# Kernel optimization log

Measured on AMD Instinct MI355X. Metric: run time of the kernel, lower is better.

The kernel has to match this reference:

```python
import jax, jax.numpy as jnp
from jax import lax
import numpy as np

_BN_SCALE = 1.0 / float(np.sqrt(1.0 + 1e-5))  # eval BN: running_mean=0, running_var=1
SEMANTIC_GROUPS = [
    ("head_spine", [0, 1, 2, 3, 20]),
    ("left_arm", [4, 5, 6, 7, 21, 22]),
    ("right_arm", [8, 9, 10, 11, 23, 24]),
    ("left_leg", [12, 13, 14, 15]),
    ("right_leg", [16, 17, 18, 19]),
]
_SKELETON_EDGES = [(3, 2), (2, 20), (20, 1), (1, 0), (20, 4), (4, 5), (5, 6), (6, 22), (6, 7), (7, 21),
                   (20, 8), (8, 9), (9, 10), (10, 24), (10, 11), (11, 23), (0, 12), (12, 13), (13, 14),
                   (14, 15), (0, 16), (16, 17), (17, 18), (18, 19)]


def _full_adj():
    adj = np.zeros((25, 25))
    for i, j in [(a - 1, b - 1) for a, b in _SKELETON_EDGES]:
        if 0 <= i < 25 and 0 <= j < 25:
            adj[i, j] = 1.0
            adj[j, i] = 1.0
    adj += np.eye(25)
    deg = adj.sum(1, keepdims=True)
    deg[deg == 0] = 1.0
    return adj / deg


def _sub_adj(joints):
    fa = _full_adj()
    sa = fa[np.ix_(joints, joints)].copy()
    n = len(joints)
    if n > 1:
        sa += np.eye(n)
        deg = sa.sum(1)
        for node in np.nonzero(deg == 1.0)[0]:
            if node != 0:
                sa[0, node] = 1.0
                sa[node, 0] = 1.0
    deg = sa.sum(1, keepdims=True)
    deg[deg == 0] = 1.0
    return jnp.asarray((sa / deg).astype(np.float32))


def _bn(y, g, b):
    # eval-mode BatchNorm2d with running stats (0, 1)
    return y * (g * _BN_SCALE)[None, :, None, None] + b[None, :, None, None]


def _st_layer(x, adj, sw, sb, tw, tb, g, b, res):
    # x: (B, Cin, T, V); sw: (3*Cout, Cin); tw: (Cout, Cout, 3, 1)
    if res is None:
        r = x
    else:
        rw, rb, rg, rbb = res
        r = _bn(jnp.einsum('oc,bctv->botv', rw, x) + rb[None, :, None, None], rg, rbb)
    xg = jnp.einsum('uv,bctv->bctu', adj, x)  # adjacency message passing
    y = jnp.einsum('oc,bctv->botv', sw, xg) + sb[None, :, None, None]
    B, oc3, T, V = y.shape
    y = y.reshape(B, 3, oc3 // 3, T, V).sum(axis=1)  # sum spatial kernel partitions
    y = lax.conv_general_dilated(y, tw, (1, 1), ((1, 1), (0, 0))) + tb[None, :, None, None]
    return jax.nn.relu(_bn(y + r, g, b))


def _vq(inp, cb):
    # inp: (B, D), cb: (K, D); straight-through VQ with commitment_cost=0.25
    d = jnp.sum(inp * inp, 1, keepdims=True) + jnp.sum(cb * cb, 1) - 2.0 * (inp @ cb.T)
    idx = jnp.argmin(d, axis=1)
    q = cb[idx]
    sg = lax.stop_gradient
    loss = jnp.mean((q - sg(inp)) ** 2) + 0.25 * jnp.mean((sg(q) - inp) ** 2)
    return inp + sg(q - inp), loss, idx


def _forward(x, embed_w, embed_b, p1, p2, p3, codebooks):
    h = jnp.einsum('btvc,oc->btvo', x, embed_w) + embed_b  # (B,T,25,64)
    h = h.transpose(0, 3, 1, 2)  # (B,64,T,25)
    quants, losses, idxs = [], [], []
    for gi, (_, joints) in enumerate(SEMANTIC_GROUPS):
        adj = _sub_adj(joints)
        y = h[:, :, :, np.asarray(joints)]
        sw1, sb1, tw1, tb1, g1, b1 = [p[gi] for p in p1]
        y = _st_layer(y, adj, sw1, sb1, tw1, tb1, g1, b1, None)
        rw2, rb2, rg2, rbb2, sw2, sb2, tw2, tb2, g2, b2 = [p[gi] for p in p2]
        y = _st_layer(y, adj, sw2, sb2, tw2, tb2, g2, b2, (rw2, rb2, rg2, rbb2))
        rw3, rb3, rg3, rbb3, sw3, sb3, tw3, tb3, g3, b3 = [p[gi] for p in p3]
        y = _st_layer(y, adj, sw3, sb3, tw3, tb3, g3, b3, (rw3, rb3, rg3, rbb3))
        feat = y.mean(axis=(2, 3))  # AdaptiveAvgPool2d((1,1))
        q, l, i = _vq(feat, codebooks[gi])
        quants.append(q)
        losses.append(l)
        idxs.append(i)
    return jnp.stack(quants), jnp.sum(jnp.stack(losses)), jnp.stack(idxs)


def setup_inputs() -> dict:
    ks = iter(jax.random.split(jax.random.key(0), 48))

    def rn(shape, scale=0.05):
        return jax.random.normal(next(ks), shape, jnp.float32) * scale

    return {
        "x": jax.random.normal(next(ks), (64, 256, 25, 3), jnp.float32),
        "embed_w": rn((64, 3), 0.3),
        "embed_b": rn((64,), 0.01),
        "sgcn_w1": rn((5, 192, 64)),
        "sgcn_b1": rn((5, 192), 0.01),
        "tconv_w1": rn((5, 64, 64, 3, 1)),
        "tconv_b1": rn((5, 64), 0.01),
        "bn_g1": jnp.ones((5, 64), jnp.float32),
        "bn_b1": jnp.zeros((5, 64), jnp.float32),
        "res_w2": rn((5, 128, 64)),
        "res_b2": rn((5, 128), 0.01),
        "resbn_g2": jnp.ones((5, 128), jnp.float32),
        "resbn_b2": jnp.zeros((5, 128), jnp.float32),
        "sgcn_w2": rn((5, 384, 64)),
        "sgcn_b2": rn((5, 384), 0.01),
        "tconv_w2": rn((5, 128, 128, 3, 1)),
        "tconv_b2": rn((5, 128), 0.01),
        "bn_g2": jnp.ones((5, 128), jnp.float32),
        "bn_b2": jnp.zeros((5, 128), jnp.float32),
        "res_w3": rn((5, 64, 128)),
        "res_b3": rn((5, 64), 0.01),
        "resbn_g3": jnp.ones((5, 64), jnp.float32),
        "resbn_b3": jnp.zeros((5, 64), jnp.float32),
        "sgcn_w3": rn((5, 192, 128)),
        "sgcn_b3": rn((5, 192), 0.01),
        "tconv_w3": rn((5, 64, 64, 3, 1)),
        "tconv_b3": rn((5, 64), 0.01),
        "bn_g3": jnp.ones((5, 64), jnp.float32),
        "bn_b3": jnp.zeros((5, 64), jnp.float32),
        "codebooks": jax.random.uniform(next(ks), (5, 128, 64), jnp.float32, -1.0 / 128, 1.0 / 128),
    }


def reference(x, embed_w, embed_b, sgcn_w1, sgcn_b1, tconv_w1, tconv_b1, bn_g1, bn_b1,
              res_w2, res_b2, resbn_g2, resbn_b2, sgcn_w2, sgcn_b2, tconv_w2, tconv_b2, bn_g2, bn_b2,
              res_w3, res_b3, resbn_g3, resbn_b3, sgcn_w3, sgcn_b3, tconv_w3, tconv_b3, bn_g3, bn_b3,
              codebooks):
    p1 = (sgcn_w1, sgcn_b1, tconv_w1, tconv_b1, bn_g1, bn_b1)
    p2 = (res_w2, res_b2, resbn_g2, resbn_b2, sgcn_w2, sgcn_b2, tconv_w2, tconv_b2, bn_g2, bn_b2)
    p3 = (res_w3, res_b3, resbn_g3, resbn_b3, sgcn_w3, sgcn_b3, tconv_w3, tconv_b3, bn_g3, bn_b3)
    return _forward(x, embed_w, embed_b, p1, p2, p3, codebooks)
```

## Files before the change

### kernel.cpp

```cpp
#include <hip/hip_runtime.h>

#define T_ 256
#define B_ 64
static constexpr float BNS = 0.9999950000374997f;

__device__ __constant__ int d_perm[25] = {0,1,2,3,20, 4,5,6,7,21,22, 8,9,10,11,23,24, 12,13,14,15, 16,17,18,19};
__device__ __constant__ int d_gstart[5] = {0,5,11,17,21};
__device__ __constant__ int d_gn[5] = {5,6,6,4,4};
__device__ __constant__ int d_edges[21][2] = {
  {2,1},{1,19},{19,0},{19,3},{3,4},{4,5},{5,21},{5,6},{6,20},{19,7},
  {7,8},{8,9},{9,23},{9,10},{10,22},{11,12},{12,13},{13,14},{15,16},{16,17},{17,18}};

__global__ void adj_kernel(float* __restrict__ adjout){
  if (threadIdx.x != 0 || blockIdx.x != 0) return;
  double fa[25][25];
  for (int i=0;i<25;i++) for (int j=0;j<25;j++) fa[i][j]=0.0;
  for (int e=0;e<21;e++){ int i=d_edges[e][0], j=d_edges[e][1]; fa[i][j]=1.0; fa[j][i]=1.0; }
  for (int i=0;i<25;i++) fa[i][i] += 1.0;
  for (int i=0;i<25;i++){
    double dg=0; for (int j=0;j<25;j++) dg += fa[i][j];
    if (dg==0.0) dg=1.0;
    for (int j=0;j<25;j++) fa[i][j] /= dg;
  }
  for (int g=0; g<5; g++){
    int n = d_gn[g]; int gs = d_gstart[g];
    for (int q=0;q<36;q++) adjout[g*36+q] = 0.f;
    double sa[6][6];
    for (int a=0;a<n;a++) for (int b=0;b<n;b++) sa[a][b] = fa[d_perm[gs+a]][d_perm[gs+b]];
    for (int a=0;a<n;a++) sa[a][a] += 1.0;
    double deg[6];
    for (int a=0;a<n;a++){ double s=0; for (int b=0;b<n;b++) s += sa[a][b]; deg[a]=s; }
    for (int a=1;a<n;a++) if (deg[a]==1.0){ sa[0][a]=1.0; sa[a][0]=1.0; }
    for (int a=0;a<n;a++){
      double s=0; for (int b=0;b<n;b++) s += sa[a][b];
      if (s==0.0) s=1.0;
      for (int b=0;b<n;b++) adjout[g*36 + a*n + b] = (float)(sa[a][b]/s);
    }
  }
}

__global__ void zero_kernel(float* __restrict__ feat, float* __restrict__ loss){
  int i = blockIdx.x*256 + threadIdx.x;
  if (i < 5*64*64) feat[i] = 0.f;
  if (i == 0) loss[0] = 0.f;
}

__global__ __launch_bounds__(256) void fold_swe(
    const float* __restrict__ sw1, const float* __restrict__ sw2, const float* __restrict__ sw3,
    float* __restrict__ swe1, float* __restrict__ swe2, float* __restrict__ swe3){
  int i = blockIdx.x*256 + threadIdx.x;
  if (i < 20480){ int g=i/4096, r=i%4096;
    swe1[i] = sw1[g*12288 + r] + sw1[g*12288 + 4096 + r] + sw1[g*12288 + 8192 + r];
  } else if (i < 61440){ int j=i-20480; int g=j/8192, r=j%8192;
    swe2[j] = sw2[g*24576 + r] + sw2[g*24576 + 8192 + r] + sw2[g*24576 + 16384 + r];
  } else if (i < 102400){ int j=i-61440; int g=j/8192, r=j%8192;
    swe3[j] = sw3[g*24576 + r] + sw3[g*24576 + 8192 + r] + sw3[g*24576 + 16384 + r];
  }
}

template<int Cm, int Cout>
__global__ __launch_bounds__(256) void transpose_tw(const float* __restrict__ tw, float* __restrict__ twT){
  int e = blockIdx.x*256 + threadIdx.x;
  if (e >= 5*3*Cm*Cout) return;
  int o = e % Cout;
  int t = e / Cout;
  int m = t % Cm; t /= Cm;
  int k = t % 3; int g = t/3;
  twT[e] = tw[(size_t)g*Cout*Cm*3 + (o*Cm+m)*3 + k];
}

template<int Cm, int Cin, int Cout>
__global__ __launch_bounds__(256) void prep_gemm(
    const float* __restrict__ twT, const float* __restrict__ swe,
    const float* __restrict__ bg, float* __restrict__ WC){
  constexpr int CT = 256/Cout;
  __shared__ float sS[Cm*CT];
  int g = blockIdx.x, k = blockIdx.y, cz = blockIdx.z;
  int tid = threadIdx.x;
  for (int i=tid; i<Cm*CT; i+=256){
    int m = i/CT, cc = i%CT;
    sS[i] = swe[(size_t)g*Cm*Cin + m*Cin + cz*CT + cc];
  }
  __syncthreads();
  int o = tid % Cout, cc = tid / Cout;
  const float* tp = twT + ((size_t)(g*3+k)*Cm)*Cout + o;
  float acc = 0.f;
  #pragma unroll 4
  for (int m=0;m<Cm;m++) acc += tp[(size_t)m*Cout]*sS[m*CT+cc];
  int c = cz*CT + cc;
  WC[(size_t)g*3*Cin*Cout + ((size_t)k*Cin + c)*Cout + o] = bg[g*Cout+o]*BNS*acc;
}

__global__ __launch_bounds__(256) void prep_rw(
    const float* __restrict__ rw2, const float* __restrict__ rg2, const float* __restrict__ bg2,
    const float* __restrict__ rw3, const float* __restrict__ rg3, const float* __restrict__ bg3,
    float* __restrict__ RW2, float* __restrict__ RW3){
  int i = blockIdx.x*256 + threadIdx.x;
  if (i < 40960){ int g=i/8192, r=i%8192, c=r>>7, o=r&127;
    RW2[i] = bg2[g*128+o]*BNS*rg2[g*128+o]*BNS*rw2[(size_t)g*8192 + o*64 + c];
  } else if (i < 81920){ int j=i-40960; int g=j/8192, r=j%8192, c=r>>6, o=r&63;
    RW3[j] = bg3[g*64+o]*BNS*rg3[g*64+o]*BNS*rw3[(size_t)g*8192 + o*128 + c];
  }
}

__global__ __launch_bounds__(128) void prep_bias(
    const float* __restrict__ twT1, const float* __restrict__ twT2, const float* __restrict__ twT3,
    const float* __restrict__ sb1, const float* __restrict__ tb1, const float* __restrict__ bg1, const float* __restrict__ bb1,
    const float* __restrict__ sb2, const float* __restrict__ tb2, const float* __restrict__ bg2, const float* __restrict__ bb2,
    const float* __restrict__ rb2, const float* __restrict__ rg2, const float* __restrict__ rbb2,
    const float* __restrict__ sb3, const float* __restrict__ tb3, const float* __restrict__ bg3, const float* __restrict__ bb3,
    const float* __restrict__ rb3, const float* __restrict__ rg3, const float* __restrict__ rbb3,
    float* __restrict__ B1, float* __restrict__ RS1, float* __restrict__ B2, float* __restrict__ B3){
  __shared__ float sbe[128];
  int g = blockIdx.x, L = blockIdx.y, tid = threadIdx.x;
  if (L == 0){
    if (tid<64) sbe[tid] = sb1[g*192+tid] + sb1[g*192+64+tid] + sb1[g*192+128+tid];
    __syncthreads();
    if (tid<64){ int o=tid; float gsc = bg1[g*64+o]*BNS;
      for (int k=0;k<3;k++){ float s=0.f; const float* tp = twT1 + ((size_t)(g*3+k)*64)*64 + o;
        for (int m=0;m<64;m++) s += tp[m*64]*sbe[m];
        B1[g*256+(k+1)*64+o] = gsc*s; }
      B1[g*256+o] = gsc*tb1[g*64+o] + bb1[g*64+o];
      RS1[g*64+o] = gsc;
    }
  } else if (L == 1){
    sbe[tid] = sb2[g*384+tid] + sb2[g*384+128+tid] + sb2[g*384+256+tid];
    __syncthreads();
    { int o=tid; float gsc = bg2[g*128+o]*BNS; float rgs = rg2[g*128+o]*BNS;
      for (int k=0;k<3;k++){ float s=0.f; const float* tp = twT2 + ((size_t)(g*3+k)*128)*128 + o;
        for (int m=0;m<128;m++) s += tp[m*128]*sbe[m];
        B2[g*512+(k+1)*128+o] = gsc*s; }
      B2[g*512+o] = gsc*(tb2[g*128+o] + rgs*rb2[g*128+o] + rbb2[g*128+o]) + bb2[g*128+o];
    }
  } else {
    if (tid<64) sbe[tid] = sb3[g*192+tid] + sb3[g*192+64+tid] + sb3[g*192+128+tid];
    __syncthreads();
    if (tid<64){ int o=tid; float gsc = bg3[g*64+o]*BNS; float rgs = rg3[g*64+o]*BNS;
      for (int k=0;k<3;k++){ float s=0.f; const float* tp = twT3 + ((size_t)(g*3+k)*64)*64 + o;
        for (int m=0;m<64;m++) s += tp[m*64]*sbe[m];
        B3[g*256+(k+1)*64+o] = gsc*s; }
      B3[g*256+o] = gsc*(tb3[g*64+o] + rgs*rb3[g*64+o] + rbb3[g*64+o]) + bb3[g*64+o];
    }
  }
}

template<int Cin, int COS, int NJ, int MODE>
__global__ __launch_bounds__(256) void st_layer(
    const float* __restrict__ in, float* __restrict__ out,
    const float* __restrict__ W, const float* __restrict__ RW,
    const float* __restrict__ BV, const float* __restrict__ RS,
    const float* __restrict__ adjg, const float* __restrict__ ew,
    const float* __restrict__ eb, int gstart)
{
  constexpr int TC = 16;
  constexpr int SE = (TC+2)*NJ;
  constexpr int SITES = TC*NJ;
  constexpr int SP = SITES/8;
  static_assert(SP == 2*NJ, "tap-merge ranges assume SP == 2*NJ (TC=16)");
  constexpr int OP = 2;
  constexpr int NCH = Cin/32;
  constexpr int G = (SP%4==0) ? 4 : 5;
  __shared__ float sIn[SE*32];
  __shared__ float sXg[SE*32];
  __shared__ float sAdj[NJ*NJ];
  __shared__ float sX3[MODE==1 ? SE*3 : 1];
  const int tid = threadIdx.x;
  const int b = blockIdx.y;
  const int t0 = blockIdx.x*TC;
  const int ooff = blockIdx.z*64;
  W += ooff; BV += ooff;
  if (MODE != 1) RW += ooff;
  if (MODE == 2) out += ooff;

  if (tid < NJ*NJ) sAdj[tid] = adjg[tid];
  if (MODE == 1){
    for (int e=tid; e<SE*3; e+=256){
      int se = e/3, j = e - se*3;
      int tl = se/NJ; int u = se - tl*NJ; int t = t0 + tl - 1;
      float v = 0.f;
      if (t>=0 && t<T_){ int joint = d_perm[gstart+u]; v = in[(((size_t)b*T_ + t)*25 + joint)*3 + j]; }
      sX3[e] = v;
    }
  }

  const int lane = tid & 63;
  const int o = lane & 31;
  const int sg = (tid>>6)*2 + (lane>>5);
  const int s0 = sg*SP;

  float acc[SP][OP];
  {
    float bno[OP], bk0[OP], bk1[OP], bk2[OP];
    #pragma unroll
    for (int j=0;j<OP;j++){ int oj = j*32 + o;
      bno[j]=BV[oj]; bk0[j]=BV[COS+oj]; bk1[j]=BV[2*COS+oj]; bk2[j]=BV[3*COS+oj]; }
    #pragma unroll
    for (int i=0;i<SP;i++){
      int s = s0 + i; int tg = t0 + s/NJ;
      #pragma unroll
      for (int j=0;j<OP;j++)
        acc[i][j] = bno[j] + bk1[j] + (tg>0 ? bk0[j] : 0.f) + (tg<T_-1 ? bk2[j] : 0.f);
    }
  }

  #pragma unroll 1
  for (int cz=0; cz<NCH; ++cz){
    __syncthreads();
    if (MODE == 1){
      int cg = cz*32 + (tid & 31);
      float w0 = ew[cg*3], w1 = ew[cg*3+1], w2 = ew[cg*3+2], b0 = eb[cg];
      for (int e=tid; e<SE*32; e+=256){
        int se = e>>5; int t = t0 + se/NJ - 1;
        float v = 0.f;
        if (t>=0 && t<T_) v = b0 + sX3[se*3]*w0 + sX3[se*3+1]*w1 + sX3[se*3+2]*w2;
        sIn[e] = v;
      }
    } else {
      for (int e4=tid; e4<SE*8; e4+=256){
        int se = e4>>3; int cc = (e4&7)<<2;
        int tl = se/NJ; int u = se - tl*NJ; int t = t0 + tl - 1;
        float4 v = make_float4(0.f,0.f,0.f,0.f);
        if (t>=0 && t<T_) v = *(const float4*)&in[(((size_t)b*T_ + t)*NJ + u)*(size_t)Cin + cz*32 + cc];
        *(float4*)&sIn[se*32+cc] = v;
      }
    }
    __syncthreads();
    for (int e=tid; e<SE*32; e+=256){
      int se = e>>5; int c = e&31; int u = se%NJ; int base = (se-u)*32 + c;
      float a = 0.f;
      #pragma unroll
      for (int v=0; v<NJ; v++) a += sAdj[u*NJ+v]*sIn[base + v*32];
      sXg[e] = a;
    }
    __syncthreads();
    #pragma unroll 1
    for (int c4=0;c4<32;c4+=4){
      const float* Wc = W + (size_t)(cz*32 + c4)*COS;
      float wv[3][4][OP];
      #pragma unroll
      for (int k=0;k<3;k++)
        #pragma unroll
        for (int q=0;q<4;q++)
          #pragma unroll
          for (int j=0;j<OP;j++)
            wv[k][q][j] = Wc[((size_t)k*Cin + q)*COS + j*32 + o];
      {
        float4 xr[NJ];
        #pragma unroll
        for (int r=0;r<NJ;r++) xr[r] = *(const float4*)&sXg[(s0+r)*32 + c4];
        #pragma unroll
        for (int r=0;r<NJ;r++)
          #pragma unroll
          for (int j=0;j<OP;j++)
            acc[r][j] += xr[r].x*wv[0][0][j] + xr[r].y*wv[0][1][j] + xr[r].z*wv[0][2][j] + xr[r].w*wv[0][3][j];
      }
      {
        float4 xr[NJ];
        #pragma unroll
        for (int r=0;r<NJ;r++) xr[r] = *(const float4*)&sXg[(s0+NJ+r)*32 + c4];
        #pragma unroll
        for (int r=0;r<NJ;r++){
          #pragma unroll
          for (int j=0;j<OP;j++)
            acc[NJ+r][j] += xr[r].x*wv[0][0][j] + xr[r].y*wv[0][1][j] + xr[r].z*wv[0][2][j] + xr[r].w*wv[0][3][j];
          #pragma unroll
          for (int j=0;j<OP;j++)
            acc[r][j] += xr[r].x*wv[1][0][j] + xr[r].y*wv[1][1][j] + xr[r].z*wv[1][2][j] + xr[r].w*wv[1][3][j];
        }
      }
      {
        float4 xr[NJ];
        #pragma unroll
        for (int r=0;r<NJ;r++) xr[r] = *(const float4*)&sXg[(s0+2*NJ+r)*32 + c4];
        #pragma unroll
        for (int r=0;r<NJ;r++){
          #pragma unroll
          for (int j=0;j<OP;j++)
            acc[NJ+r][j] += xr[r].x*wv[1][0][j] + xr[r].y*wv[1][1][j] + xr[r].z*wv[1][2][j] + xr[r].w*wv[1][3][j];
          #pragma unroll
          for (int j=0;j<OP;j++)
            acc[r][j] += xr[r].x*wv[2][0][j] + xr[r].y*wv[2][1][j] + xr[r].z*wv[2][2][j] + xr[r].w*wv[2][3][j];
        }
      }
      {
        float4 xr[NJ];
        #pragma unroll
        for (int r=0;r<NJ;r++) xr[r] = *(const float4*)&sXg[(s0+3*NJ+r)*32 + c4];
        #pragma unroll
        for (int r=0;r<NJ;r++)
          #pragma unroll
          for (int j=0;j<OP;j++)
            acc[NJ+r][j] += xr[r].x*wv[2][0][j] + xr[r].y*wv[2][1][j] + xr[r].z*wv[2][2][j] + xr[r].w*wv[2][3][j];
      }
    }
    if (MODE == 1){
      float rsv = RS[cz*32 + o];
      if (cz == 0){
        #pragma unroll
        for (int i0=0;i0<SP;i0+=G){
          float xr[G];
          #pragma unroll
          for (int u=0;u<G;u++) xr[u] = sIn[(s0+i0+u+NJ)*32 + o];
          #pragma unroll
          for (int u=0;u<G;u++) acc[i0+u][0] += xr[u]*rsv;
        }
      } else {
        #pragma unroll
        for (int i0=0;i0<SP;i0+=G){
          float xr[G];
          #pragma unroll
          for (int u=0;u<G;u++) xr[u] = sIn[(s0+i0+u+NJ)*32 + o];
          #pragma unroll
          for (int u=0;u<G;u++) acc[i0+u][1] += xr[u]*rsv;
        }
      }
    } else {
      #pragma unroll 1
      for (int c4=0;c4<32;c4+=4){
        float rv[4][OP];
        #pragma unroll
        for (int q=0;q<4;q++)
          #pragma unroll
          for (int j=0;j<OP;j++) rv[q][j] = RW[(size_t)(cz*32+c4+q)*COS + j*32 + o];
        #pragma unroll
        for (int i0=0;i0<SP;i0+=G){
          float4 xr[G];
          #pragma unroll
          for (int u=0;u<G;u++)
            xr[u] = *(const float4*)&sIn[(s0+i0+u+NJ)*32 + c4];
          #pragma unroll
          for (int u=0;u<G;u++)
            #pragma unroll
            for (int j=0;j<OP;j++)
              acc[i0+u][j] += xr[u].x*rv[0][j] + xr[u].y*rv[1][j] + xr[u].z*rv[2][j] + xr[u].w*rv[3][j];
        }
      }
    }
  }
  if (MODE == 3){
    #pragma unroll
    for (int j=0;j<OP;j++){
      float sum = 0.f;
      #pragma unroll
      for (int i=0;i<SP;i++) sum += fmaxf(acc[i][j], 0.f);
      atomicAdd(&out[(size_t)b*64 + j*32 + o], sum);
    }
  } else {
    size_t obase = ((size_t)b*T_ + t0)*NJ*COS;
    #pragma unroll
    for (int i=0;i<SP;i++)
      #pragma unroll
      for (int j=0;j<OP;j++)
        out[obase + (size_t)(s0+i)*COS + j*32 + o] = fmaxf(acc[i][j], 0.f);
  }
}

__global__ __launch_bounds__(128) void vq_kernel(const float* __restrict__ feat,
    const float* __restrict__ cb, float* __restrict__ dout){
  int b = blockIdx.x, g = blockIdx.y, tid = threadIdx.x;
  __shared__ float sF[64];
  __shared__ float sD[128]; __shared__ int sI[128];
  __shared__ float sL[64];
  float inv = 1.0f/(256.0f*(float)d_gn[g]);
  if (tid < 64) sF[tid] = feat[((size_t)g*64 + b)*64 + tid]*inv;
  __syncthreads();
  const float* cbg = cb + (size_t)g*128*64;
  {
    const float* c = cbg + (size_t)tid*64;
    float d = 0.f;
    for (int i=0;i<64;i++){ float df = c[i]-sF[i]; d += df*df; }
    sD[tid] = d; sI[tid] = tid;
  }
  __syncthreads();
  for (int s=64; s>0; s>>=1){
    if (tid < s){
      float d2 = sD[tid+s]; int i2 = sI[tid+s];
      if (d2 < sD[tid] || (d2 == sD[tid] && i2 < sI[tid])){ sD[tid]=d2; sI[tid]=i2; }
    }
    __syncthreads();
  }
  int idx = sI[0];
  if (tid < 64){
    float q = cbg[(size_t)idx*64 + tid];
    dout[((size_t)g*64 + b)*64 + tid] = q;
    float df = q - sF[tid];
    sL[tid] = df*df;
  }
  __syncthreads();
  if (tid == 0){
    float s = 0.f;
    for (int i=0;i<64;i++) s += sL[i];
    atomicAdd(dout + 20480, 1.25f*s/4096.0f);
    dout[20481 + g*64 + b] = (float)idx;
  }
}

static void launch_st1(int nj, hipStream_t s, const float* x, float* A1,
    const float* WC, const float* BV, const float* RS, const float* adj,
    const float* ew, const float* eb, int gstart){
  dim3 grid(T_/16, B_, 1);
  switch(nj){
    case 4: st_layer<64,64,4,1><<<grid,256,0,s>>>(x,A1,WC,nullptr,BV,RS,adj,ew,eb,gstart); break;
    case 5: st_layer<64,64,5,1><<<grid,256,0,s>>>(x,A1,WC,nullptr,BV,RS,adj,ew,eb,gstart); break;
    case 6: st_layer<64,64,6,1><<<grid,256,0,s>>>(x,A1,WC,nullptr,BV,RS,adj,ew,eb,gstart); break;
  }
}
static void launch_st2(int nj, hipStream_t s, const float* A1, float* A2,
    const float* WC, const float* RW, const float* BV, const float* adj){
  dim3 grid(T_/16, B_, 2);
  switch(nj){
    case 4: st_layer<64,128,4,2><<<grid,256,0,s>>>(A1,A2,WC,RW,BV,nullptr,adj,nullptr,nullptr,0); break;
    case 5: st_layer<64,128,5,2><<<grid,256,0,s>>>(A1,A2,WC,RW,BV,nullptr,adj,nullptr,nullptr,0); break;
    case 6: st_layer<64,128,6,2><<<grid,256,0,s>>>(A1,A2,WC,RW,BV,nullptr,adj,nullptr,nullptr,0); break;
  }
}
static void launch_st3(int nj, hipStream_t s, const float* A2, float* featg,
    const float* WC, const float* RW, const float* BV, const float* adj){
  dim3 grid(T_/16, B_, 1);
  switch(nj){
    case 4: st_layer<128,64,4,3><<<grid,256,0,s>>>(A2,featg,WC,RW,BV,nullptr,adj,nullptr,nullptr,0); break;
    case 5: st_layer<128,64,5,3><<<grid,256,0,s>>>(A2,featg,WC,RW,BV,nullptr,adj,nullptr,nullptr,0); break;
    case 6: st_layer<128,64,6,3><<<grid,256,0,s>>>(A2,featg,WC,RW,BV,nullptr,adj,nullptr,nullptr,0); break;
  }
}

extern "C" void kernel_launch(void* const* d_in, const int* in_sizes, int n_in,
                              void* d_out, int out_size, void* d_ws, size_t ws_size,
                              hipStream_t stream) {
  const float* x    = (const float*)d_in[0];
  const float* ew   = (const float*)d_in[1];
  const float* eb   = (const float*)d_in[2];
  const float* sw1  = (const float*)d_in[3];
  const float* sb1  = (const float*)d_in[4];
  const float* tw1  = (const float*)d_in[5];
  const float* tb1  = (const float*)d_in[6];
  const float* bg1  = (const float*)d_in[7];
  const float* bb1  = (const float*)d_in[8];
  const float* rw2  = (const float*)d_in[9];
  const float* rb2  = (const float*)d_in[10];
  const float* rg2  = (const float*)d_in[11];
  const float* rbb2 = (const float*)d_in[12];
  const float* sw2  = (const float*)d_in[13];
  const float* sb2  = (const float*)d_in[14];
  const float* tw2  = (const float*)d_in[15];
  const float* tb2  = (const float*)d_in[16];
  const float* bg2  = (const float*)d_in[17];
  const float* bb2  = (const float*)d_in[18];
  const float* rw3  = (const float*)d_in[19];
  const float* rb3  = (const float*)d_in[20];
  const float* rg3  = (const float*)d_in[21];
  const float* rbb3 = (const float*)d_in[22];
  const float* sw3  = (const float*)d_in[23];
  const float* sb3  = (const float*)d_in[24];
  const float* tw3  = (const float*)d_in[25];
  const float* tb3  = (const float*)d_in[26];
  const float* bg3  = (const float*)d_in[27];
  const float* bb3  = (const float*)d_in[28];
  const float* cbs  = (const float*)d_in[29];
  float* dout = (float*)d_out;
  float* ws = (float*)d_ws;

  const size_t OFF_ADJ = 0;
  const size_t OFF_WC1 = 256;
  const size_t OFF_B1  = 61696;
  const size_t OFF_RS1 = 62976;
  const size_t OFF_WC2 = 63296;
  const size_t OFF_RW2 = 186176;
  const size_t OFF_B2  = 227136;
  const size_t OFF_WC3 = 229696;
  const size_t OFF_RW3 = 352576;
  const size_t OFF_B3  = 393536;
  const size_t OFF_FEAT= 394816;
  const size_t OFF_A1  = 415296;
  const size_t OFF_A2  = 6706752;
  const size_t WS_FLOATS = 19289664;
  if (ws_size < WS_FLOATS*sizeof(float)) return;

  float* adj5 = ws + OFF_ADJ;
  float* WC1  = ws + OFF_WC1;  float* B1 = ws + OFF_B1;  float* RS1 = ws + OFF_RS1;
  float* WC2  = ws + OFF_WC2;  float* RW2 = ws + OFF_RW2; float* B2 = ws + OFF_B2;
  float* WC3  = ws + OFF_WC3;  float* RW3 = ws + OFF_RW3; float* B3 = ws + OFF_B3;
  float* feat = ws + OFF_FEAT;
  float* A1   = ws + OFF_A1;
  float* A2   = ws + OFF_A2;

  float* twT1 = A2;
  float* twT2 = A2 + 61440;
  float* twT3 = A2 + 307200;
  float* swe1 = A2 + 368640;
  float* swe2 = A2 + 389120;
  float* swe3 = A2 + 430080;

  zero_kernel<<<80, 256, 0, stream>>>(feat, dout + 20480);
  adj_kernel<<<1, 64, 0, stream>>>(adj5);
  fold_swe<<<400, 256, 0, stream>>>(sw1, sw2, sw3, swe1, swe2, swe3);
  transpose_tw<64,64>  <<<240, 256, 0, stream>>>(tw1, twT1);
  transpose_tw<128,128><<<960, 256, 0, stream>>>(tw2, twT2);
  transpose_tw<64,64>  <<<240, 256, 0, stream>>>(tw3, twT3);
  prep_gemm<64,64,64>  <<<dim3(5,3,16), 256, 0, stream>>>(twT1, swe1, bg1, WC1);
  prep_gemm<128,64,128><<<dim3(5,3,32), 256, 0, stream>>>(twT2, swe2, bg2, WC2);
  prep_gemm<64,128,64> <<<dim3(5,3,32), 256, 0, stream>>>(twT3, swe3, bg3, WC3);
  prep_rw<<<320, 256, 0, stream>>>(rw2, rg2, bg2, rw3, rg3, bg3, RW2, RW3);
  prep_bias<<<dim3(5,3), 128, 0, stream>>>(twT1, twT2, twT3,
      sb1, tb1, bg1, bb1,
      sb2, tb2, bg2, bb2, rb2, rg2, rbb2,
      sb3, tb3, bg3, bb3, rb3, rg3, rbb3,
      B1, RS1, B2, B3);

  const int h_gn[5] = {5,6,6,4,4};
  const int h_gstart[5] = {0,5,11,17,21};
  for (int g=0; g<5; g++){
    int nj = h_gn[g];
    launch_st1(nj, stream, x, A1, WC1 + (size_t)g*12288, B1 + g*256, RS1 + g*64,
               adj5 + g*36, ew, eb, h_gstart[g]);
    launch_st2(nj, stream, A1, A2, WC2 + (size_t)g*24576, RW2 + (size_t)g*8192,
               B2 + g*512, adj5 + g*36);
    launch_st3(nj, stream, A2, feat + (size_t)g*4096, WC3 + (size_t)g*24576,
               RW3 + (size_t)g*8192, B3 + g*256, adj5 + g*36);
  }
  vq_kernel<<<dim3(B_,5), 128, 0, stream>>>(feat, cbs, dout);
}
```

Baseline: 1.535 ms.

## Apply adjacency after channel GEMM in registers, drop sXg staging pass

Reorders the computation so the spatial-temporal weights multiply the raw input tile first, and the per-group adjacency is applied afterwards to the register accumulators (matrix multiplication is associative). This removes the shared-memory sXg buffer, the adjacency pre-pass and one barrier per channel chunk. The residual 1x1 projection is fused into the main tap loop with its own accumulator. The cost is a second accumulator array, which raises register pressure, plus an NJ×NJ mix in the epilogue.

```diff
diff --git a/kernel.cpp b/kernel.cpp
--- a/kernel.cpp
+++ b/kernel.cpp
@@ -156,12 +156,10 @@
   constexpr int SE = (TC+2)*NJ;
   constexpr int SITES = TC*NJ;
   constexpr int SP = SITES/8;
-  static_assert(SP == 2*NJ, "tap-merge ranges assume SP == 2*NJ (TC=16)");
+  static_assert(SP == 2*NJ, "structure assumes SP == 2*NJ (TC=16)");
   constexpr int OP = 2;
   constexpr int NCH = Cin/32;
-  constexpr int G = (SP%4==0) ? 4 : 5;
   __shared__ float sIn[SE*32];
-  __shared__ float sXg[SE*32];
   __shared__ float sAdj[NJ*NJ];
   __shared__ float sX3[MODE==1 ? SE*3 : 1];
   const int tid = threadIdx.x;
@@ -188,7 +186,8 @@
   const int sg = (tid>>6)*2 + (lane>>5);
   const int s0 = sg*SP;
 
-  float acc[SP][OP];
+  float acc_y[SP][OP];
+  float acc_r[SP][OP];
   {
     float bno[OP], bk0[OP], bk1[OP], bk2[OP];
     #pragma unroll
@@ -198,8 +197,10 @@
     for (int i=0;i<SP;i++){
       int s = s0 + i; int tg = t0 + s/NJ;
       #pragma unroll
-      for (int j=0;j<OP;j++)
-        acc[i][j] = bno[j] + bk1[j] + (tg>0 ? bk0[j] : 0.f) + (tg<T_-1 ? bk2[j] : 0.f);
+      for (int j=0;j<OP;j++){
+        acc_y[i][j] = 0.f;
+        acc_r[i][j] = bno[j] + bk1[j] + (tg>0 ? bk0[j] : 0.f) + (tg<T_-1 ? bk2[j] : 0.f);
+      }
     }
   }
 
@@ -225,14 +226,6 @@
       }
     }
     __syncthreads();
-    for (int e=tid; e<SE*32; e+=256){
-      int se = e>>5; int c = e&31; int u = se%NJ; int base = (se-u)*32 + c;
-      float a = 0.f;
-      #pragma unroll
-      for (int v=0; v<NJ; v++) a += sAdj[u*NJ+v]*sIn[base + v*32];
-      sXg[e] = a;
-    }
-    __syncthreads();
     #pragma unroll 1
     for (int c4=0;c4<32;c4+=4){
       const float* Wc = W + (size_t)(cz*32 + c4)*COS;
@@ -244,114 +237,125 @@
           #pragma unroll
           for (int j=0;j<OP;j++)
             wv[k][q][j] = Wc[((size_t)k*Cin + q)*COS + j*32 + o];
+      float rv[4][OP];
+      if (MODE != 1){
+        #pragma unroll
+        for (int q=0;q<4;q++)
+          #pragma unroll
+          for (int j=0;j<OP;j++) rv[q][j] = RW[(size_t)(cz*32+c4+q)*COS + j*32 + o];
+      }
       {
         float4 xr[NJ];
         #pragma unroll
-        for (int r=0;r<NJ;r++) xr[r] = *(const float4*)&sXg[(s0+r)*32 + c4];
+        for (int r=0;r<NJ;r++) xr[r] = *(const float4*)&sIn[(s0+r)*32 + c4];
         #pragma unroll
         for (int r=0;r<NJ;r++)
           #pragma unroll
           for (int j=0;j<OP;j++)
-            acc[r][j] += xr[r].x*wv[0][0][j] + xr[r].y*wv[0][1][j] + xr[r].z*wv[0][2][j] + xr[r].w*wv[0][3][j];
+            acc_y[r][j] += xr[r].x*wv[0][0][j] + xr[r].y*wv[0][1][j] + xr[r].z*wv[0][2][j] + xr[r].w*wv[0][3][j];
       }
       {
         float4 xr[NJ];
         #pragma unroll
-        for (int r=0;r<NJ;r++) xr[r] = *(const float4*)&sXg[(s0+NJ+r)*32 + c4];
+        for (int r=0;r<NJ;r++) xr[r] = *(const float4*)&sIn[(s0+NJ+r)*32 + c4];
         #pragma unroll
         for (int r=0;r<NJ;r++){
           #pragma unroll
           for (int j=0;j<OP;j++)
-            acc[NJ+r][j] += xr[r].x*wv[0][0][j] + xr[r].y*wv[0][1][j] + xr[r].z*wv[0][2][j] + xr[r].w*wv[0][3][j];
-          #pragma unroll
-          for (int j=0;j<OP;j++)
-            acc[r][j] += xr[r].x*wv[1][0][j] + xr[r].y*wv[1][1][j] + xr[r].z*wv[1][2][j] + xr[r].w*wv[1][3][j];
+            acc_y[NJ+r][j] += xr[r].x*wv[0][0][j] + xr[r].y*wv[0][1][j] + xr[r].z*wv[0][2][j] + xr[r].w*wv[0][3][j];
+          #pragma unroll
+          for (int j=0;j<OP;j++)
+            acc_y[r][j] += xr[r].x*wv[1][0][j] + xr[r].y*wv[1][1][j] + xr[r].z*wv[1][2][j] + xr[r].w*wv[1][3][j];
+          if (MODE != 1){
+            #pragma unroll
+            for (int j=0;j<OP;j++)
+              acc_r[r][j] += xr[r].x*rv[0][j] + xr[r].y*rv[1][j] + xr[r].z*rv[2][j] + xr[r].w*rv[3][j];
+          }
         }
       }
       {
         float4 xr[NJ];
         #pragma unroll
-        for (int r=0;r<NJ;r++) xr[r] = *(const float4*)&sXg[(s0+2*NJ+r)*32 + c4];
+        for (int r=0;r<NJ;r++) xr[r] = *(const float4*)&sIn[(s0+2*NJ+r)*32 + c4];
         #pragma unroll
         for (int r=0;r<NJ;r++){
           #pragma unroll
           for (int j=0;j<OP;j++)
-            acc[NJ+r][j] += xr[r].x*wv[1][0][j] + xr[r].y*wv[1][1][j] + xr[r].z*wv[1][2][j] + xr[r].w*wv[1][3][j];
-          #pragma unroll
-          for (int j=0;j<OP;j++)
-            acc[r][j] += xr[r].x*wv[2][0][j] + xr[r].y*wv[2][1][j] + xr[r].z*wv[2][2][j] + xr[r].w*wv[2][3][j];
+            acc_y[NJ+r][j] += xr[r].x*wv[1][0][j] + xr[r].y*wv[1][1][j] + xr[r].z*wv[1][2][j] + xr[r].w*wv[1][3][j];
+          #pragma unroll
+          for (int j=0;j<OP;j++)
+            acc_y[r][j] += xr[r].x*wv[2][0][j] + xr[r].y*wv[2][1][j] + xr[r].z*wv[2][2][j] + xr[r].w*wv[2][3][j];
+          if (MODE != 1){
+            #pragma unroll
+            for (int j=0;j<OP;j++)
+              acc_r[NJ+r][j] += xr[r].x*rv[0][j] + xr[r].y*rv[1][j] + xr[r].z*rv[2][j] + xr[r].w*rv[3][j];
+          }
         }
       }
       {
         float4 xr[NJ];
         #pragma unroll
-        for (int r=0;r<NJ;r++) xr[r] = *(const float4*)&sXg[(s0+3*NJ+r)*32 + c4];
+        for (int r=0;r<NJ;r++) xr[r] = *(const float4*)&sIn[(s0+3*NJ+r)*32 + c4];
         #pragma unroll
         for (int r=0;r<NJ;r++)
           #pragma unroll
           for (int j=0;j<OP;j++)
-            acc[NJ+r][j] += xr[r].x*wv[2][0][j] + xr[r].y*wv[2][1][j] + xr[r].z*wv[2][2][j] + xr[r].w*wv[2][3][j];
+            acc_y[NJ+r][j] += xr[r].x*wv[2][0][j] + xr[r].y*wv[2][1][j] + xr[r].z*wv[2][2][j] + xr[r].w*wv[2][3][j];
       }
     }
     if (MODE == 1){
       float rsv = RS[cz*32 + o];
       if (cz == 0){
         #pragma unroll
-        for (int i0=0;i0<SP;i0+=G){
-          float xr[G];
-          #pragma unroll
-          for (int u=0;u<G;u++) xr[u] = sIn[(s0+i0+u+NJ)*32 + o];
-          #pragma unroll
-          for (int u=0;u<G;u++) acc[i0+u][0] += xr[u]*rsv;
+        for (int i=0;i<SP;i++) acc_r[i][0] += sIn[(s0+i+NJ)*32 + o]*rsv;
+      } else {
+        #pragma unroll
+        for (int i=0;i<SP;i++) acc_r[i][1] += sIn[(s0+i+NJ)*32 + o]*rsv;
+      }
+    }
+  }
+  if (MODE == 3){
+    float sum[OP];
+    #pragma unroll
+    for (int j=0;j<OP;j++) sum[j] = 0.f;
+    #pragma unroll
+    for (int tt=0;tt<2;tt++)
+      #pragma unroll
+      for (int u=0;u<NJ;u++){
+        float val[OP];
+        #pragma unroll
+        for (int j=0;j<OP;j++) val[j] = acc_r[tt*NJ+u][j];
+        #pragma unroll
+        for (int v=0;v<NJ;v++){
+          float a = sAdj[u*NJ+v];
+          #pragma unroll
+          for (int j=0;j<OP;j++) val[j] += a*acc_y[tt*NJ+v][j];
         }
-      } else {
-        #pragma unroll
-        for (int i0=0;i0<SP;i0+=G){
-          float xr[G];
-          #pragma unroll
-          for (int u=0;u<G;u++) xr[u] = sIn[(s0+i0+u+NJ)*32 + o];
-          #pragma unroll
-          for (int u=0;u<G;u++) acc[i0+u][1] += xr[u]*rsv;
-        }
-      }
-    } else {
-      #pragma unroll 1
-      for (int c4=0;c4<32;c4+=4){
-        float rv[4][OP];
-        #pragma unroll
-        for (int q=0;q<4;q++)
-          #pragma unroll
-          for (int j=0;j<OP;j++) rv[q][j] = RW[(size_t)(cz*32+c4+q)*COS + j*32 + o];
-        #pragma unroll
-        for (int i0=0;i0<SP;i0+=G){
-          float4 xr[G];
-          #pragma unroll
-          for (int u=0;u<G;u++)
-            xr[u] = *(const float4*)&sIn[(s0+i0+u+NJ)*32 + c4];
-          #pragma unroll
-          for (int u=0;u<G;u++)
-            #pragma unroll
-            for (int j=0;j<OP;j++)
-              acc[i0+u][j] += xr[u].x*rv[0][j] + xr[u].y*rv[1][j] + xr[u].z*rv[2][j] + xr[u].w*rv[3][j];
-        }
-      }
-    }
-  }
-  if (MODE == 3){
+        #pragma unroll
+        for (int j=0;j<OP;j++) sum[j] += fmaxf(val[j], 0.f);
+      }
     #pragma unroll
-    for (int j=0;j<OP;j++){
-      float sum = 0.f;
-      #pragma unroll
-      for (int i=0;i<SP;i++) sum += fmaxf(acc[i][j], 0.f);
-      atomicAdd(&out[(size_t)b*64 + j*32 + o], sum);
-    }
+    for (int j=0;j<OP;j++)
+      atomicAdd(&out[(size_t)b*64 + j*32 + o], sum[j]);
   } else {
     size_t obase = ((size_t)b*T_ + t0)*NJ*COS;
     #pragma unroll
-    for (int i=0;i<SP;i++)
+    for (int tt=0;tt<2;tt++)
       #pragma unroll
-      for (int j=0;j<OP;j++)
-        out[obase + (size_t)(s0+i)*COS + j*32 + o] = fmaxf(acc[i][j], 0.f);
+      for (int u=0;u<NJ;u++){
+        float val[OP];
+        #pragma unroll
+        for (int j=0;j<OP;j++) val[j] = acc_r[tt*NJ+u][j];
+        #pragma unroll
+        for (int v=0;v<NJ;v++){
+          float a = sAdj[u*NJ+v];
+          #pragma unroll
+          for (int j=0;j<OP;j++) val[j] += a*acc_y[tt*NJ+v][j];
+        }
+        #pragma unroll
+        for (int j=0;j<OP;j++)
+          out[obase + (size_t)(s0+tt*NJ+u)*COS + j*32 + o] = fmaxf(val[j], 0.f);
+      }
   }
 }
 
```

After: 1.618 ms. +5.4%, slower.
